# Performance work log

Measured on AMD Instinct MI355X. Metric: run time of the kernel, lower is better.

The kernel has to match this reference:

```python
import jax, jax.numpy as jnp
import numpy as np

N, E, B, C, L, HLS = 30000, 480000, 64, 128, 3, 64
PARAM_NAMES = ['Wq','bq','Wk','bk','Wv','bv','Wskip','bskip','lstm_Wih_f','lstm_Whh_f','lstm_bih_f','lstm_bhh_f','lstm_Wih_b','lstm_Whh_b','lstm_bih_b','lstm_bhh_b','att_W','att_b','gP_W1','gP_b1','gP_W2','gP_b2','gT_W1','gT_b1','gT_W2','gT_b2','m_W0','m_b0','m_W1','m_b1','m_W2','m_b2']


def setup_inputs() -> dict:
    key = jax.random.key(0)
    ks = iter(jax.random.split(key, 64))
    rn = lambda shape: jax.random.normal(next(ks), shape, dtype=jnp.float32) * 0.05
    inp = {
        'x': jax.random.normal(next(ks), (N, C), dtype=jnp.float32),
        'edge_index': jax.random.randint(next(ks), (2, E), 0, N, dtype=jnp.int32),
        'batch': jnp.sort(jax.random.randint(next(ks), (N,), 0, B, dtype=jnp.int32)),
        'hls_attr': jax.random.normal(next(ks), (B, HLS), dtype=jnp.float32),
        'Wq': rn((L, C, C)), 'bq': rn((L, C)),
        'Wk': rn((L, C, C)), 'bk': rn((L, C)),
        'Wv': rn((L, C, C)), 'bv': rn((L, C)),
        'Wskip': rn((L, C, C)), 'bskip': rn((L, C)),
        'lstm_Wih_f': rn((4 * C, C)), 'lstm_Whh_f': rn((4 * C, C)),
        'lstm_bih_f': rn((4 * C,)), 'lstm_bhh_f': rn((4 * C,)),
        'lstm_Wih_b': rn((4 * C, C)), 'lstm_Whh_b': rn((4 * C, C)),
        'lstm_bih_b': rn((4 * C,)), 'lstm_bhh_b': rn((4 * C,)),
        'att_W': rn((2 * C, 1)), 'att_b': rn((1,)),
        'gP_W1': rn((C, C)), 'gP_b1': rn((C,)), 'gP_W2': rn((C, 1)), 'gP_b2': rn((1,)),
        'gT_W1': rn((C, C)), 'gT_b1': rn((C,)), 'gT_W2': rn((C, 1)), 'gT_b2': rn((1,)),
        'm_W0': rn((2 * C + HLS, 64)), 'm_b0': rn((64,)),
        'm_W1': rn((64, 64)), 'm_b1': rn((64,)),
        'm_W2': rn((64, 1)), 'm_b2': rn((1,)),
    }
    return inp


def _segment_softmax(logits, seg, num):
    m = jax.ops.segment_max(logits, seg, num_segments=num)
    e = jnp.exp(logits - m[seg])
    d = jax.ops.segment_sum(e, seg, num_segments=num)
    return e / d[seg]


def _lstm(xs, Wih, Whh, bih, bhh):
    # xs: [L, N, C] -> outputs [L, N, H]
    H = Whh.shape[1]
    h0 = jnp.zeros((xs.shape[1], H), xs.dtype)
    bias = bih + bhh
    def step(carry, xt):
        h, c = carry
        z = xt @ Wih.T + h @ Whh.T + bias
        i, f, g, o = jnp.split(z, 4, axis=-1)
        c = jax.nn.sigmoid(f) * c + jax.nn.sigmoid(i) * jnp.tanh(g)
        h = jax.nn.sigmoid(o) * jnp.tanh(c)
        return (h, c), h
    _, hs = jax.lax.scan(step, (h0, h0), xs)
    return hs


def _gate_pool(x, batch, W1, b1, W2, b2):
    gate = jax.nn.relu(x @ W1 + b1) @ W2 + b2          # [N, 1]
    gate = _segment_softmax(gate[:, 0], batch, B)[:, None]
    return jax.ops.segment_sum(gate * x, batch, num_segments=B)


def _forward(x, edge_index, batch, hls_attr, Wq, bq, Wk, bk, Wv, bv, Wskip, bskip,
             lstm_Wih_f, lstm_Whh_f, lstm_bih_f, lstm_bhh_f,
             lstm_Wih_b, lstm_Whh_b, lstm_bih_b, lstm_bhh_b,
             att_W, att_b, gP_W1, gP_b1, gP_W2, gP_b2, gT_W1, gT_b1, gT_W2, gT_b2,
             m_W0, m_b0, m_W1, m_b1, m_W2, m_b2):
    src, dst = edge_index[0], edge_index[1]
    scale = 1.0 / jnp.sqrt(jnp.asarray(C, jnp.float32))
    h_list = []
    for i in range(L):
        q = x @ Wq[i] + bq[i]
        k = x @ Wk[i] + bk[i]
        v = x @ Wv[i] + bv[i]
        logits = jnp.sum(q[dst] * k[src], axis=-1) * scale   # [E]
        alpha = _segment_softmax(logits, dst, N)             # per-dst softmax
        agg = jax.ops.segment_sum(alpha[:, None] * v[src], dst, num_segments=N)
        x = jax.nn.relu(agg + x @ Wskip[i] + bskip[i])       # TransformerConv + root skip, then ReLU
        h_list.append(x)
    xs = jnp.stack(h_list)                                   # [L, N, C]
    hf = _lstm(xs, lstm_Wih_f, lstm_Whh_f, lstm_bih_f, lstm_bhh_f)
    hb = _lstm(xs[::-1], lstm_Wih_b, lstm_Whh_b, lstm_bih_b, lstm_bhh_b)[::-1]
    hcat = jnp.concatenate([hf, hb], axis=-1)                # [L, N, 2C]
    a = jax.nn.softmax((hcat @ att_W)[..., 0] + att_b[0], axis=0)  # softmax over layers
    x = jnp.sum(a[..., None] * xs, axis=0)                   # [N, C] JK-LSTM output
    out_P = _gate_pool(x, batch, gP_W1, gP_b1, gP_W2, gP_b2)
    out_T = _gate_pool(x, batch, gT_W1, gT_b1, gT_W2, gT_b2)
    h = jnp.concatenate([out_P, out_T, hls_attr], axis=-1)   # [B, 2C+HLS]
    h = jax.nn.relu(h @ m_W0 + m_b0)
    h = jax.nn.relu(h @ m_W1 + m_b1)
    return h @ m_W2 + m_b2                                   # [B, 1]


def reference(x, edge_index, batch, hls_attr, Wq, bq, Wk, bk, Wv, bv, Wskip, bskip,
              lstm_Wih_f, lstm_Whh_f, lstm_bih_f, lstm_bhh_f,
              lstm_Wih_b, lstm_Whh_b, lstm_bih_b, lstm_bhh_b,
              att_W, att_b, gP_W1, gP_b1, gP_W2, gP_b2, gT_W1, gT_b1, gT_W2, gT_b2,
              m_W0, m_b0, m_W1, m_b1, m_W2, m_b2):
    return _forward(x, edge_index, batch, hls_attr, Wq, bq, Wk, bk, Wv, bv, Wskip, bskip,
                    lstm_Wih_f, lstm_Whh_f, lstm_bih_f, lstm_bhh_f,
                    lstm_Wih_b, lstm_Whh_b, lstm_bih_b, lstm_bhh_b,
                    att_W, att_b, gP_W1, gP_b1, gP_W2, gP_b2, gT_W1, gT_b1, gT_W2, gT_b2,
                    m_W0, m_b0, m_W1, m_b1, m_W2, m_b2)
```

## Files before the change

### kernel.cpp

```cpp
#include <hip/hip_runtime.h>
#include <math.h>

#define NN 30000
#define EE 480000
#define BB 64
#define CC 128
#define LLAYERS 3
#define HLSD 64

typedef __attribute__((ext_vector_type(8))) short bf16x8;
typedef __attribute__((ext_vector_type(4))) float f32x4;

__device__ inline unsigned short f2bf(float f){
  unsigned u = __float_as_uint(f);
  u += 0x7fffu + ((u >> 16) & 1u);
  return (unsigned short)(u >> 16);
}
__device__ inline float bf2f(unsigned short h){
  return __uint_as_float(((unsigned)h) << 16);
}

__global__ void k_hist(const int* __restrict__ dst, int* __restrict__ counts, int E){
  int e = blockIdx.x*256 + threadIdx.x;
  if (e < E) atomicAdd(&counts[dst[e]], 1);
}
__global__ void k_scan_block(const int* __restrict__ counts, int* __restrict__ row_ptr,
                             int* __restrict__ bsums, int n){
  __shared__ int sm[256];
  int i = blockIdx.x*256 + threadIdx.x;
  int v = (i < n) ? counts[i] : 0;
  sm[threadIdx.x] = v; __syncthreads();
  for (int off = 1; off < 256; off <<= 1){
    int t = (threadIdx.x >= off) ? sm[threadIdx.x - off] : 0;
    __syncthreads();
    sm[threadIdx.x] += t;
    __syncthreads();
  }
  if (i < n) row_ptr[i+1] = sm[threadIdx.x];
  if (threadIdx.x == 255) bsums[blockIdx.x] = sm[255];
}
__global__ void k_scan_bsums(const int* __restrict__ bsums, int* __restrict__ bexcl, int nb){
  if (threadIdx.x == 0 && blockIdx.x == 0){
    int s = 0;
    for (int i = 0; i < nb; i++){ int t = bsums[i]; bexcl[i] = s; s += t; }
  }
}
__global__ void k_scan_add(int* __restrict__ row_ptr, const int* __restrict__ bexcl, int n){
  int i = blockIdx.x*256 + threadIdx.x;
  if (i < n) row_ptr[i+1] += bexcl[i >> 8];
  if (i == 0) row_ptr[0] = 0;
}
__global__ void k_fill(const int* __restrict__ src, const int* __restrict__ dst,
                       const int* __restrict__ row_ptr, int* __restrict__ fill,
                       int* __restrict__ esrc, int E){
  int e = blockIdx.x*256 + threadIdx.x;
  if (e < E){
    int d = dst[e];
    int pos = row_ptr[d] + atomicAdd(&fill[d], 1);
    esrc[pos] = src[e];
  }
}

struct PrepPtrs {
  const float* tsrc[14]; unsigned short* tdst[14];
  const float* csrc[4];  unsigned short* cdst[4];
  const float *bihf, *bhhf, *bihb, *bhhb;
  float *cbf, *cbb;
};
__global__ __launch_bounds__(256) void k_prep(PrepPtrs p){
  int b = blockIdx.x, tid = threadIdx.x;
  if (b < 14){
    const float* s = p.tsrc[b]; unsigned short* d = p.tdst[b];
    for (int i = tid; i < 16384; i += 256){
      int k = i >> 7, n = i & 127;
      d[n*128 + k] = f2bf(s[i]);
    }
  } else if (b < 30){
    int m = (b - 14) >> 2, ch = (b - 14) & 3;
    const float* s = p.csrc[m] + ch*16384; unsigned short* d = p.cdst[m] + ch*16384;
    for (int i = tid; i < 16384; i += 256) d[i] = f2bf(s[i]);
  } else {
    for (int i = tid; i < 512; i += 256){
      p.cbf[i] = p.bihf[i] + p.bhhf[i];
      p.cbb[i] = p.bihb[i] + p.bhhb[i];
    }
  }
}
__global__ __launch_bounds__(256) void k_cvt_x(const float* __restrict__ src,
                                               unsigned short* __restrict__ dst, int n8){
  int i = blockIdx.x*256 + threadIdx.x;
  if (i >= n8) return;
  float4 a = *(const float4*)(src + (size_t)i*8);
  float4 b = *(const float4*)(src + (size_t)i*8 + 4);
  union { unsigned short u[8]; uint4 v; } o;
  o.u[0]=f2bf(a.x); o.u[1]=f2bf(a.y); o.u[2]=f2bf(a.z); o.u[3]=f2bf(a.w);
  o.u[4]=f2bf(b.x); o.u[5]=f2bf(b.y); o.u[6]=f2bf(b.z); o.u[7]=f2bf(b.w);
  *(uint4*)(dst + (size_t)i*8) = o.v;
}

struct Quad { const unsigned short* Bt[4]; const float* bias[4]; };

template<int RELU, int OUTBF16>
__global__ __launch_bounds__(256) void k_mfma_gemm(
    const unsigned short* __restrict__ A0, Quad qd,
    float* __restrict__ Cf, unsigned short* __restrict__ Cb,
    int M, int ldC, int colsPerMat)
{
  __shared__ unsigned short As0[64*128];
  __shared__ unsigned short Bs0[64*128];

  const int tid = threadIdx.x;
  const int row0 = blockIdx.x*64;
  const int colg0 = blockIdx.y*64;
  const int mi = colg0 / colsPerMat;
  const int nloc = colg0 - mi*colsPerMat;
  const unsigned short* Bt0 = qd.Bt[mi];

  #pragma unroll
  for (int i = 0; i < 4; i++){
    int ch = tid + i*256;
    int r = ch >> 4, c16 = ch & 15;
    int gr = row0 + r;
    uint4 av = make_uint4(0,0,0,0);
    if (gr < M) av = *(const uint4*)(A0 + (size_t)gr*128 + c16*8);
    *(uint4*)((char*)As0 + ((r*256 + c16*16) ^ ((r&7)<<4))) = av;
    uint4 bv = *(const uint4*)(Bt0 + (size_t)(nloc + r)*128 + c16*8);
    *(uint4*)((char*)Bs0 + ((r*256 + c16*16) ^ ((r&7)<<4))) = bv;
  }
  __syncthreads();

  const int w = tid >> 6, l = tid & 63;
  const int lr = l & 15, lhi = l >> 4;

  f32x4 acc[4];
  #pragma unroll
  for (int f = 0; f < 4; f++){ acc[f][0]=0.f; acc[f][1]=0.f; acc[f][2]=0.f; acc[f][3]=0.f; }

  #pragma unroll
  for (int kt = 0; kt < 4; kt++){
    int arow = w*16 + lr;
    bf16x8 a = *(const bf16x8*)((const char*)As0 + ((arow*256 + kt*64 + lhi*16) ^ ((arow&7)<<4)));
    #pragma unroll
    for (int f = 0; f < 4; f++){
      int brow = f*16 + lr;
      bf16x8 b = *(const bf16x8*)((const char*)Bs0 + ((brow*256 + kt*64 + lhi*16) ^ ((brow&7)<<4)));
      acc[f] = __builtin_amdgcn_mfma_f32_16x16x32_bf16(a, b, acc[f], 0, 0, 0);
    }
  }

  const float* bias = qd.bias[mi];
  #pragma unroll
  for (int f = 0; f < 4; f++){
    int colg = colg0 + f*16 + lr;
    float bv = bias ? bias[nloc + f*16 + lr] : 0.f;
    #pragma unroll
    for (int r = 0; r < 4; r++){
      int grow = row0 + w*16 + lhi*4 + r;
      if (grow < M){
        float v = acc[f][r] + bv;
        if (RELU) v = fmaxf(v, 0.f);
        if (OUTBF16) Cb[(size_t)grow*ldC + colg] = f2bf(v);
        else         Cf[(size_t)grow*ldC + colg] = v;
      }
    }
  }
}

template<int FIRST>
__global__ __launch_bounds__(256) void k_lstm_fused(
    const unsigned short* __restrict__ X,
    const unsigned short* __restrict__ H,
    const unsigned short* __restrict__ Wih,
    const unsigned short* __restrict__ Whh,
    const float* __restrict__ cbias,
    unsigned short* __restrict__ Hout,
    float* __restrict__ Cst,
    float* __restrict__ score,
    const float* __restrict__ attW,
    int M)
{
  __shared__ unsigned short As[64*128];
  __shared__ unsigned short Bs[128*128];
  const int tid = threadIdx.x;
  const int row0 = blockIdx.x*64;
  const int t0 = blockIdx.y*32;
  const int w = tid >> 6, l = tid & 63, lr = l & 15, lhi = l >> 4;

  f32x4 acc[8];
  #pragma unroll
  for (int f = 0; f < 8; f++){ acc[f][0]=0.f; acc[f][1]=0.f; acc[f][2]=0.f; acc[f][3]=0.f; }

  const int npair = FIRST ? 1 : 2;
  for (int pair = 0; pair < npair; pair++){
    const unsigned short* A  = pair ? H   : X;
    const unsigned short* Bt = pair ? Whh : Wih;
    if (pair) __syncthreads();
    #pragma unroll
    for (int i = 0; i < 4; i++){
      int ch = tid + i*256;
      int r = ch >> 4, c16 = ch & 15;
      int gr = row0 + r;
      uint4 av = make_uint4(0,0,0,0);
      if (gr < M) av = *(const uint4*)(A + (size_t)gr*128 + c16*8);
      *(uint4*)((char*)As + ((r*256 + c16*16) ^ ((r&7)<<4))) = av;
    }
    #pragma unroll
    for (int i = 0; i < 8; i++){
      int ch = tid + i*256;
      int r = ch >> 4, c16 = ch & 15;
      int gr = (r >> 5)*128 + t0 + (r & 31);
      uint4 bv = *(const uint4*)(Bt + (size_t)gr*128 + c16*8);
      *(uint4*)((char*)Bs + ((r*256 + c16*16) ^ ((r&7)<<4))) = bv;
    }
    __syncthreads();
    #pragma unroll
    for (int kt = 0; kt < 4; kt++){
      int arow = w*16 + lr;
      bf16x8 a = *(const bf16x8*)((const char*)As + ((arow*256 + kt*64 + lhi*16) ^ ((arow&7)<<4)));
      #pragma unroll
      for (int f = 0; f < 8; f++){
        int brow = f*16 + lr;
        bf16x8 b = *(const bf16x8*)((const char*)Bs + ((brow*256 + kt*64 + lhi*16) ^ ((brow&7)<<4)));
        acc[f] = __builtin_amdgcn_mfma_f32_16x16x32_bf16(a, b, acc[f], 0, 0, 0);
      }
    }
  }

  float sc[4] = {0.f, 0.f, 0.f, 0.f};
  #pragma unroll
  for (int cb = 0; cb < 2; cb++){
    int t = t0 + cb*16 + lr;
    float aw  = attW[t];
    float bi  = cbias[t];
    float bf_ = cbias[128 + t];
    float bg  = cbias[256 + t];
    float bo  = cbias[384 + t];
    #pragma unroll
    for (int r = 0; r < 4; r++){
      int grow = row0 + w*16 + lhi*4 + r;
      if (grow < M){
        float zi = acc[0+cb][r] + bi;
        float zf = acc[2+cb][r] + bf_;
        float zg = acc[4+cb][r] + bg;
        float zo = acc[6+cb][r] + bo;
        float cp = FIRST ? 0.f : Cst[(size_t)grow*128 + t];
        float si = 1.f/(1.f + expf(-zi));
        float sf = 1.f/(1.f + expf(-zf));
        float so = 1.f/(1.f + expf(-zo));
        float cn = sf*cp + si*tanhf(zg);
        float hn = so*tanhf(cn);
        Cst[(size_t)grow*128 + t] = cn;
        Hout[(size_t)grow*128 + t] = f2bf(hn);
        sc[r] += hn * aw;
      }
    }
  }
  #pragma unroll
  for (int r = 0; r < 4; r++){
    float p = sc[r];
    p += __shfl_xor(p, 1, 64);
    p += __shfl_xor(p, 2, 64);
    p += __shfl_xor(p, 4, 64);
    p += __shfl_xor(p, 8, 64);
    if (lr == 0){
      int grow = row0 + w*16 + lhi*4 + r;
      if (grow < M) atomicAdd(&score[grow], p);
    }
  }
}

__global__ __launch_bounds__(256) void k_attn(
    const unsigned short* __restrict__ qkvs, const int* __restrict__ row_ptr,
    const int* __restrict__ esrc, unsigned short* __restrict__ xout, int n)
{
  int wid = threadIdx.x >> 6, lane = threadIdx.x & 63;
  int dst = blockIdx.x*4 + wid;
  if (dst >= n) return;
  const size_t drow = (size_t)dst*512;
  ushort2 qu = *(const ushort2*)(qkvs + drow + lane*2);
  float qx = bf2f(qu.x), qy = bf2f(qu.y);
  int rs = row_ptr[dst], re = row_ptr[dst+1];
  const float scale = 0.08838834764831845f;
  float m = -INFINITY, den = 0.f, ax = 0.f, ay = 0.f;
  int e = rs;
  for (; e + 4 <= re; e += 4){
    int s0 = esrc[e], s1 = esrc[e+1], s2 = esrc[e+2], s3 = esrc[e+3];
    const unsigned short* r0 = qkvs + (size_t)s0*512;
    const unsigned short* r1 = qkvs + (size_t)s1*512;
    const unsigned short* r2 = qkvs + (size_t)s2*512;
    const unsigned short* r3 = qkvs + (size_t)s3*512;
    ushort2 k0 = *(const ushort2*)(r0 + 128 + lane*2);
    ushort2 k1 = *(const ushort2*)(r1 + 128 + lane*2);
    ushort2 k2 = *(const ushort2*)(r2 + 128 + lane*2);
    ushort2 k3 = *(const ushort2*)(r3 + 128 + lane*2);
    ushort2 v0 = *(const ushort2*)(r0 + 256 + lane*2);
    ushort2 v1 = *(const ushort2*)(r1 + 256 + lane*2);
    ushort2 v2 = *(const ushort2*)(r2 + 256 + lane*2);
    ushort2 v3 = *(const ushort2*)(r3 + 256 + lane*2);
    float d0 = qx*bf2f(k0.x) + qy*bf2f(k0.y);
    float d1 = qx*bf2f(k1.x) + qy*bf2f(k1.y);
    float d2 = qx*bf2f(k2.x) + qy*bf2f(k2.y);
    float d3 = qx*bf2f(k3.x) + qy*bf2f(k3.y);
    #pragma unroll
    for (int o = 1; o < 64; o <<= 1){
      d0 += __shfl_xor(d0, o, 64);
      d1 += __shfl_xor(d1, o, 64);
      d2 += __shfl_xor(d2, o, 64);
      d3 += __shfl_xor(d3, o, 64);
    }
    float l0 = d0*scale, l1 = d1*scale, l2 = d2*scale, l3 = d3*scale;
    float bm = fmaxf(fmaxf(l0, l1), fmaxf(l2, l3));
    if (bm > m){
      float rr = expf(m - bm);
      den *= rr; ax *= rr; ay *= rr; m = bm;
    }
    float w0 = expf(l0 - m), w1 = expf(l1 - m), w2 = expf(l2 - m), w3 = expf(l3 - m);
    den += (w0 + w1) + (w2 + w3);
    ax += w0*bf2f(v0.x) + w1*bf2f(v1.x) + w2*bf2f(v2.x) + w3*bf2f(v3.x);
    ay += w0*bf2f(v0.y) + w1*bf2f(v1.y) + w2*bf2f(v2.y) + w3*bf2f(v3.y);
  }
  for (; e < re; ++e){
    int s = esrc[e];
    const unsigned short* sr = qkvs + (size_t)s*512;
    ushort2 kk = *(const ushort2*)(sr + 128 + lane*2);
    ushort2 vv = *(const ushort2*)(sr + 256 + lane*2);
    float d = qx*bf2f(kk.x) + qy*bf2f(kk.y);
    #pragma unroll
    for (int o = 1; o < 64; o <<= 1) d += __shfl_xor(d, o, 64);
    float logit = d * scale;
    if (logit > m){
      float rr = expf(m - logit);
      den *= rr; ax *= rr; ay *= rr; m = logit;
    }
    float wgt = expf(logit - m);
    den += wgt; ax += wgt*bf2f(vv.x); ay += wgt*bf2f(vv.y);
  }
  ushort2 sku = *(const ushort2*)(qkvs + drow + 384 + lane*2);
  float ox = 0.f, oy = 0.f;
  if (re > rs){ ox = ax/den; oy = ay/den; }
  ox = fmaxf(ox + bf2f(sku.x), 0.f); oy = fmaxf(oy + bf2f(sku.y), 0.f);
  ushort2 o2; o2.x = f2bf(ox); o2.y = f2bf(oy);
  *(ushort2*)(xout + (size_t)dst*128 + lane*2) = o2;
}

__global__ void k_jk_weights(const float* __restrict__ sF, const float* __restrict__ sB,
                             const float* __restrict__ attb, float* __restrict__ a, int n){
  int i = blockIdx.x*256 + threadIdx.x;
  if (i >= n) return;
  float s0 = sF[i]       + sB[i]       + attb[0];
  float s1 = sF[n+i]     + sB[n+i]     + attb[0];
  float s2 = sF[2*n+i]   + sB[2*n+i]   + attb[0];
  float mm = fmaxf(s0, fmaxf(s1, s2));
  float e0 = expf(s0-mm), e1 = expf(s1-mm), e2 = expf(s2-mm);
  float d = e0 + e1 + e2;
  a[i] = e0/d; a[n+i] = e1/d; a[2*n+i] = e2/d;
}
__global__ void k_jk_combine(const float* __restrict__ a,
                             const unsigned short* __restrict__ x0,
                             const unsigned short* __restrict__ x1,
                             const unsigned short* __restrict__ x2,
                             float* __restrict__ xjk, unsigned short* __restrict__ xjkb, int n){
  int idx = blockIdx.x*256 + threadIdx.x;
  if (idx >= n*128) return;
  int node = idx >> 7;
  float r = a[node]     * bf2f(x0[idx])
          + a[n+node]   * bf2f(x1[idx])
          + a[2*n+node] * bf2f(x2[idx]);
  xjk[idx] = r;
  xjkb[idx] = f2bf(r);
}

__global__ __launch_bounds__(256) void k_rowdot(const unsigned short* __restrict__ g,
                                                const float* __restrict__ w2,
                                                const float* __restrict__ b2, float* __restrict__ out, int n){
  int wid = threadIdx.x >> 6, lane = threadIdx.x & 63;
  int node = blockIdx.x*4 + wid;
  if (node >= n) return;
  ushort2 gv = *(const ushort2*)(g + (size_t)node*128 + lane*2);
  float2 wv = *(const float2*)(w2 + lane*2);
  float p = bf2f(gv.x)*wv.x + bf2f(gv.y)*wv.y;
  #pragma unroll
  for (int o = 1; o < 64; o <<= 1) p += __shfl_xor(p, o, 64);
  if (lane == 0) out[node] = p + b2[0];
}

__global__ void k_segbounds(const int* __restrict__ batch, int* __restrict__ segp, int n){
  int i = blockIdx.x*256 + threadIdx.x;
  if (i >= n) return;
  int b = batch[i];
  int bp = (i == 0) ? -1 : batch[i-1];
  for (int s = bp+1; s <= b; s++) segp[s] = i;
  if (i == n-1){
    for (int s = b+1; s <= BB; s++) segp[s] = n;
  }
}

__global__ __launch_bounds__(256) void k_seg_stats(
    const float* __restrict__ glP, const float* __restrict__ glT,
    const int* __restrict__ segp, float4* __restrict__ stats)
{
  const int b = blockIdx.x, tid = threadIdx.x;
  const int s0 = segp[b], s1 = segp[b+1];
  __shared__ float sred[8];

  float mP = -INFINITY, mT = -INFINITY;
  for (int i = s0 + tid; i < s1; i += 256){
    mP = fmaxf(mP, glP[i]);
    mT = fmaxf(mT, glT[i]);
  }
  #pragma unroll
  for (int o = 1; o < 64; o <<= 1){
    mP = fmaxf(mP, __shfl_xor(mP, o, 64));
    mT = fmaxf(mT, __shfl_xor(mT, o, 64));
  }
  if ((tid & 63) == 0){ sred[(tid >> 6)*2] = mP; sred[(tid >> 6)*2 + 1] = mT; }
  __syncthreads();
  mP = fmaxf(fmaxf(sred[0], sred[2]), fmaxf(sred[4], sred[6]));
  mT = fmaxf(fmaxf(sred[1], sred[3]), fmaxf(sred[5], sred[7]));
  __syncthreads();

  float dP = 0.f, dT = 0.f;
  for (int i = s0 + tid; i < s1; i += 256){
    dP += expf(glP[i] - mP);
    dT += expf(glT[i] - mT);
  }
  #pragma unroll
  for (int o = 1; o < 64; o <<= 1){
    dP += __shfl_xor(dP, o, 64);
    dT += __shfl_xor(dT, o, 64);
  }
  if ((tid & 63) == 0){ sred[(tid >> 6)*2] = dP; sred[(tid >> 6)*2 + 1] = dT; }
  __syncthreads();
  if (tid == 0){
    dP = sred[0] + sred[2] + sred[4] + sred[6];
    dT = sred[1] + sred[3] + sred[5] + sred[7];
    float4 st;
    st.x = mP; st.y = mT;
    st.z = (dP > 0.f) ? 1.f/dP : 0.f;
    st.w = (dT > 0.f) ? 1.f/dT : 0.f;
    stats[b] = st;
  }
}

__global__ __launch_bounds__(256) void k_poolsum(
    const float* __restrict__ xjk, const int* __restrict__ segp,
    const float* __restrict__ glP, const float* __restrict__ glT,
    const float4* __restrict__ stats,
    float* __restrict__ poolP, float* __restrict__ poolT)
{
  const int b = blockIdx.x;
  const int s0 = segp[b], s1 = segp[b+1];
  const float4 st = stats[b];
  const int half = threadIdx.x >> 7, c = threadIdx.x & 127;
  const int stream = blockIdx.y*2 + half;
  float aP = 0.f, aT = 0.f;
  for (int i = s0 + stream; i < s1; i += 32){
    float eP = expf(glP[i] - st.x);
    float eT = expf(glT[i] - st.y);
    float xv = xjk[(size_t)i*128 + c];
    aP += eP*xv; aT += eT*xv;
  }
  if (aP != 0.f) atomicAdd(&poolP[(size_t)b*128 + c], aP*st.z);
  if (aT != 0.f) atomicAdd(&poolT[(size_t)b*128 + c], aT*st.w);
}

__global__ __launch_bounds__(64) void k_mlp(
    const float* __restrict__ poolP, const float* __restrict__ poolT, const float* __restrict__ hls,
    const float* __restrict__ W0, const float* __restrict__ b0,
    const float* __restrict__ W1, const float* __restrict__ b1,
    const float* __restrict__ W2, const float* __restrict__ b2, float* __restrict__ out)
{
  __shared__ float hin[320];
  __shared__ float h1[64];
  int b = blockIdx.x, j = threadIdx.x;
  for (int i = j; i < 320; i += 64){
    float vv;
    if (i < 128)      vv = poolP[(size_t)b*128 + i];
    else if (i < 256) vv = poolT[(size_t)b*128 + (i-128)];
    else              vv = hls[(size_t)b*64 + (i-256)];
    hin[i] = vv;
  }
  __syncthreads();
  float s = b0[j];
  for (int kk = 0; kk < 320; kk++) s += hin[kk] * W0[kk*64 + j];
  h1[j] = fmaxf(s, 0.f);
  __syncthreads();
  float s2 = b1[j];
  for (int kk = 0; kk < 64; kk++) s2 += h1[kk] * W1[kk*64 + j];
  float h2 = fmaxf(s2, 0.f);
  float p = h2 * W2[j];
  #pragma unroll
  for (int o = 1; o < 64; o <<= 1) p += __shfl_xor(p, o, 64);
  if (j == 0) out[b] = p + b2[0];
}

extern "C" void kernel_launch(void* const* d_in, const int* in_sizes, int n_in,
                              void* d_out, int out_size, void* d_ws, size_t ws_size,
                              hipStream_t stream)
{
  (void)in_sizes; (void)n_in; (void)out_size; (void)ws_size;
  const int N = NN, E = EE, C = CC;
  const float* x     = (const float*)d_in[0];
  const int*   ei    = (const int*)d_in[1];
  const int*   batch = (const int*)d_in[2];
  const float* hls   = (const float*)d_in[3];
  const float* Wq = (const float*)d_in[4],  *bq = (const float*)d_in[5];
  const float* Wk = (const float*)d_in[6],  *bk = (const float*)d_in[7];
  const float* Wv = (const float*)d_in[8],  *bv = (const float*)d_in[9];
  const float* Ws = (const float*)d_in[10], *bs = (const float*)d_in[11];
  const float* Wih_f = (const float*)d_in[12], *Whh_f = (const float*)d_in[13];
  const float* bih_f = (const float*)d_in[14], *bhh_f = (const float*)d_in[15];
  const float* Wih_b = (const float*)d_in[16], *Whh_b = (const float*)d_in[17];
  const float* bih_b = (const float*)d_in[18], *bhh_b = (const float*)d_in[19];
  const float* attW  = (const float*)d_in[20], *attb  = (const float*)d_in[21];
  const float* gPW1 = (const float*)d_in[22], *gPb1 = (const float*)d_in[23];
  const float* gPW2 = (const float*)d_in[24], *gPb2 = (const float*)d_in[25];
  const float* gTW1 = (const float*)d_in[26], *gTb1 = (const float*)d_in[27];
  const float* gTW2 = (const float*)d_in[28], *gTb2 = (const float*)d_in[29];
  const float* mW0 = (const float*)d_in[30], *mb0 = (const float*)d_in[31];
  const float* mW1 = (const float*)d_in[32], *mb1 = (const float*)d_in[33];
  const float* mW2 = (const float*)d_in[34], *mb2 = (const float*)d_in[35];
  float* out = (float*)d_out;

  const int* esrc_in = ei;
  const int* edst_in = ei + E;

  typedef unsigned short u16;

  char* ws = (char*)d_ws;
  size_t off = 0;
  auto alloc = [&](size_t bytes) -> char* {
    char* p = ws + off;
    off += (bytes + 255) & ~(size_t)255;
    return p;
  };
  u16* qkvsb   = (u16*)alloc((size_t)N*512*2);
  u16* xb      = (u16*)alloc((size_t)N*C*2);
  u16* xsb0    = (u16*)alloc((size_t)N*C*2);
  u16* xsb1    = (u16*)alloc((size_t)N*C*2);
  u16* xsb2    = (u16*)alloc((size_t)N*C*2);
  u16* hbA     = (u16*)alloc((size_t)N*C*2);
  u16* hbB     = (u16*)alloc((size_t)N*C*2);
  float* cbuf  = (float*)alloc((size_t)N*C*4);
  float* scores= (float*)alloc((size_t)6*N*4);
  float* ajk   = (float*)alloc((size_t)3*N*4);
  float* xjk   = (float*)alloc((size_t)N*C*4);
  u16* xjkb    = (u16*)alloc((size_t)N*C*2);
  u16* g1P     = (u16*)alloc((size_t)N*C*2);
  u16* g1T     = (u16*)alloc((size_t)N*C*2);
  int* counts  = (int*)alloc((size_t)N*4);
  int* row_ptr = (int*)alloc((size_t)(N+1)*4);
  int* bsums   = (int*)alloc(512);
  int* bexcl   = (int*)alloc(512);
  int* esrc    = (int*)alloc((size_t)E*4);
  float* glP   = (float*)alloc((size_t)N*4);
  float* glT   = (float*)alloc((size_t)N*4);
  int* segp    = (int*)alloc((size_t)(BB+1)*4);
  float* poolP = (float*)alloc((size_t)BB*C*4);
  float* poolT = (float*)alloc((size_t)BB*C*4);
  float4* sstats = (float4*)alloc((size_t)BB*16);
  u16* wT      = (u16*)alloc((size_t)14*16384*2);
  u16* wLSTM   = (u16*)alloc((size_t)4*65536*2);
  float* combF = (float*)alloc(512*4);
  float* combB = (float*)alloc(512*4);

  float* scF = scores;
  float* scB = scores + (size_t)3*N;

  u16* wTq = wT;
  u16* wTk = wT + 3*16384;
  u16* wTv = wT + 6*16384;
  u16* wTs = wT + 9*16384;
  u16* wTgP = wT + 12*16384;
  u16* wTgT = wT + 13*16384;
  u16* wIHf = wLSTM;
  u16* wHHf = wLSTM + 65536;
  u16* wIHb = wLSTM + 2*65536;
  u16* wHHb = wLSTM + 3*65536;

  const int NB  = (N + 255)/256;
  const int EBL = (E + 255)/256;

  PrepPtrs pp;
  for (int l = 0; l < 3; l++){
    pp.tsrc[l]   = Wq + (size_t)l*16384;  pp.tdst[l]   = wTq + (size_t)l*16384;
    pp.tsrc[3+l] = Wk + (size_t)l*16384;  pp.tdst[3+l] = wTk + (size_t)l*16384;
    pp.tsrc[6+l] = Wv + (size_t)l*16384;  pp.tdst[6+l] = wTv + (size_t)l*16384;
    pp.tsrc[9+l] = Ws + (size_t)l*16384;  pp.tdst[9+l] = wTs + (size_t)l*16384;
  }
  pp.tsrc[12] = gPW1; pp.tdst[12] = wTgP;
  pp.tsrc[13] = gTW1; pp.tdst[13] = wTgT;
  pp.csrc[0] = Wih_f; pp.cdst[0] = wIHf;
  pp.csrc[1] = Whh_f; pp.cdst[1] = wHHf;
  pp.csrc[2] = Wih_b; pp.cdst[2] = wIHb;
  pp.csrc[3] = Whh_b; pp.cdst[3] = wHHb;
  pp.bihf = bih_f; pp.bhhf = bhh_f; pp.bihb = bih_b; pp.bhhb = bhh_b;
  pp.cbf = combF; pp.cbb = combB;
  k_prep<<<31, 256, 0, stream>>>(pp);
  k_cvt_x<<<(N*C/8 + 255)/256, 256, 0, stream>>>(x, xb, N*C/8);

  hipMemsetAsync(counts, 0, (size_t)N*4, stream);
  k_hist<<<EBL, 256, 0, stream>>>(edst_in, counts, E);
  k_scan_block<<<NB, 256, 0, stream>>>(counts, row_ptr, bsums, N);
  k_scan_bsums<<<1, 64, 0, stream>>>(bsums, bexcl, NB);
  k_scan_add<<<NB, 256, 0, stream>>>(row_ptr, bexcl, N);
  hipMemsetAsync(counts, 0, (size_t)N*4, stream);
  k_fill<<<EBL, 256, 0, stream>>>(esrc_in, edst_in, row_ptr, counts, esrc, E);

  const int GX = (N + 63)/64;
  dim3 blk(256);

  u16* xsb[3] = {xsb0, xsb1, xsb2};
  const u16* ain = xb;
  for (int l = 0; l < LLAYERS; l++){
    Quad q;
    q.Bt[0] = wTq + (size_t)l*16384;  q.bias[0] = bq + (size_t)l*C;
    q.Bt[1] = wTk + (size_t)l*16384;  q.bias[1] = bk + (size_t)l*C;
    q.Bt[2] = wTv + (size_t)l*16384;  q.bias[2] = bv + (size_t)l*C;
    q.Bt[3] = wTs + (size_t)l*16384;  q.bias[3] = bs + (size_t)l*C;
    k_mfma_gemm<0,1><<<dim3(GX,8), blk, 0, stream>>>(ain, q, nullptr, qkvsb, N, 512, 128);
    k_attn<<<(N+3)/4, 256, 0, stream>>>(qkvsb, row_ptr, esrc, xsb[l], N);
    ain = xsb[l];
  }

  hipMemsetAsync(scores, 0, (size_t)6*N*4, stream);
  {
    u16* hbuf2[2] = {hbA, hbB};
    for (int t = 0; t < 3; t++){
      u16* hout = hbuf2[t & 1];
      u16* hin2 = hbuf2[(t & 1) ^ 1];
      if (t == 0)
        k_lstm_fused<1><<<dim3(GX,4), blk, 0, stream>>>(xsb[t], nullptr, wIHf, nullptr, combF,
                                                        hout, cbuf, scF + (size_t)t*N, attW, N);
      else
        k_lstm_fused<0><<<dim3(GX,4), blk, 0, stream>>>(xsb[t], hin2, wIHf, wHHf, combF,
                                                        hout, cbuf, scF + (size_t)t*N, attW, N);
    }
    for (int s = 0; s < 3; s++){
      int t = 2 - s;
      u16* hout = hbuf2[s & 1];
      u16* hin2 = hbuf2[(s & 1) ^ 1];
      if (s == 0)
        k_lstm_fused<1><<<dim3(GX,4), blk, 0, stream>>>(xsb[t], nullptr, wIHb, nullptr, combB,
                                                        hout, cbuf, scB + (size_t)t*N, attW + 128, N);
      else
        k_lstm_fused<0><<<dim3(GX,4), blk, 0, stream>>>(xsb[t], hin2, wIHb, wHHb, combB,
                                                        hout, cbuf, scB + (size_t)t*N, attW + 128, N);
    }
  }

  k_jk_weights<<<NB, 256, 0, stream>>>(scF, scB, attb, ajk, N);
  k_jk_combine<<<(N*C + 255)/256, 256, 0, stream>>>(ajk, xsb0, xsb1, xsb2, xjk, xjkb, N);

  {
    Quad qp; qp.Bt[0]=wTgP; qp.bias[0]=gPb1; qp.Bt[1]=nullptr; qp.bias[1]=nullptr; qp.Bt[2]=nullptr; qp.bias[2]=nullptr; qp.Bt[3]=nullptr; qp.bias[3]=nullptr;
    k_mfma_gemm<1,1><<<dim3(GX,2), blk, 0, stream>>>(xjkb, qp, nullptr, g1P, N, 128, 128);
    k_rowdot<<<(N+3)/4, 256, 0, stream>>>(g1P, gPW2, gPb2, glP, N);
    Quad qt; qt.Bt[0]=wTgT; qt.bias[0]=gTb1; qt.Bt[1]=nullptr; qt.bias[1]=nullptr; qt.Bt[2]=nullptr; qt.bias[2]=nullptr; qt.Bt[3]=nullptr; qt.bias[3]=nullptr;
    k_mfma_gemm<1,1><<<dim3(GX,2), blk, 0, stream>>>(xjkb, qt, nullptr, g1T, N, 128, 128);
    k_rowdot<<<(N+3)/4, 256, 0, stream>>>(g1T, gTW2, gTb2, glT, N);
  }

  k_segbounds<<<NB, 256, 0, stream>>>(batch, segp, N);
  k_seg_stats<<<BB, 256, 0, stream>>>(glP, glT, segp, sstats);
  hipMemsetAsync(poolP, 0, (size_t)2*BB*C*4, stream);
  k_poolsum<<<dim3(BB,16), 256, 0, stream>>>(xjk, segp, glP, glT, sstats, poolP, poolT);

  k_mlp<<<BB, 64, 0, stream>>>(poolP, poolT, hls, mW0, mb0, mW1, mb1, mW2, mb2, out);
}
```

Measured before the change: 545.4 us.

## Split attention wavefront into four edge groups with 16-byte vector loads

The per-destination attention kernel now splits each 64-lane wavefront into four 16-lane groups. Each group handles every fourth edge, with each lane loading 8 bf16 channels in one 16-byte access. Each group keeps its own online softmax state, software-prefetches the next edge's K/V rows, uses exp2 with a prescaled logit, and merges the partial softmax states across groups with shuffles at the end. This cuts the dot-product shuffle reduction from 6 steps to 4 per edge and issues wider memory accesses, at the cost of more registers and a cross-group merge.

```diff
diff --git a/kernel.cpp b/kernel.cpp
--- a/kernel.cpp
+++ b/kernel.cpp
@@ -276,71 +276,85 @@
   int wid = threadIdx.x >> 6, lane = threadIdx.x & 63;
   int dst = blockIdx.x*4 + wid;
   if (dst >= n) return;
+  const int g = lane >> 4, j = lane & 15;
   const size_t drow = (size_t)dst*512;
-  ushort2 qu = *(const ushort2*)(qkvs + drow + lane*2);
-  float qx = bf2f(qu.x), qy = bf2f(qu.y);
-  int rs = row_ptr[dst], re = row_ptr[dst+1];
-  const float scale = 0.08838834764831845f;
-  float m = -INFINITY, den = 0.f, ax = 0.f, ay = 0.f;
-  int e = rs;
-  for (; e + 4 <= re; e += 4){
-    int s0 = esrc[e], s1 = esrc[e+1], s2 = esrc[e+2], s3 = esrc[e+3];
-    const unsigned short* r0 = qkvs + (size_t)s0*512;
-    const unsigned short* r1 = qkvs + (size_t)s1*512;
-    const unsigned short* r2 = qkvs + (size_t)s2*512;
-    const unsigned short* r3 = qkvs + (size_t)s3*512;
-    ushort2 k0 = *(const ushort2*)(r0 + 128 + lane*2);
-    ushort2 k1 = *(const ushort2*)(r1 + 128 + lane*2);
-    ushort2 k2 = *(const ushort2*)(r2 + 128 + lane*2);
-    ushort2 k3 = *(const ushort2*)(r3 + 128 + lane*2);
-    ushort2 v0 = *(const ushort2*)(r0 + 256 + lane*2);
-    ushort2 v1 = *(const ushort2*)(r1 + 256 + lane*2);
-    ushort2 v2 = *(const ushort2*)(r2 + 256 + lane*2);
-    ushort2 v3 = *(const ushort2*)(r3 + 256 + lane*2);
-    float d0 = qx*bf2f(k0.x) + qy*bf2f(k0.y);
-    float d1 = qx*bf2f(k1.x) + qy*bf2f(k1.y);
-    float d2 = qx*bf2f(k2.x) + qy*bf2f(k2.y);
-    float d3 = qx*bf2f(k3.x) + qy*bf2f(k3.y);
-    #pragma unroll
-    for (int o = 1; o < 64; o <<= 1){
-      d0 += __shfl_xor(d0, o, 64);
-      d1 += __shfl_xor(d1, o, 64);
-      d2 += __shfl_xor(d2, o, 64);
-      d3 += __shfl_xor(d3, o, 64);
-    }
-    float l0 = d0*scale, l1 = d1*scale, l2 = d2*scale, l3 = d3*scale;
-    float bm = fmaxf(fmaxf(l0, l1), fmaxf(l2, l3));
-    if (bm > m){
-      float rr = expf(m - bm);
-      den *= rr; ax *= rr; ay *= rr; m = bm;
-    }
-    float w0 = expf(l0 - m), w1 = expf(l1 - m), w2 = expf(l2 - m), w3 = expf(l3 - m);
-    den += (w0 + w1) + (w2 + w3);
-    ax += w0*bf2f(v0.x) + w1*bf2f(v1.x) + w2*bf2f(v2.x) + w3*bf2f(v3.x);
-    ay += w0*bf2f(v0.y) + w1*bf2f(v1.y) + w2*bf2f(v2.y) + w3*bf2f(v3.y);
-  }
-  for (; e < re; ++e){
+
+  bf16x8 qv = *(const bf16x8*)(qkvs + drow + j*8);
+  float qf[8];
+  #pragma unroll
+  for (int i = 0; i < 8; i++) qf[i] = bf2f((unsigned short)qv[i]);
+
+  const int rs = row_ptr[dst], re = row_ptr[dst+1];
+  const float scale2 = 0.08838834764831845f * 1.4426950408889634f;
+  float m = -INFINITY, den = 0.f;
+  float acc[8];
+  #pragma unroll
+  for (int i = 0; i < 8; i++) acc[i] = 0.f;
+
+  int e = rs + g;
+  if (e < re){
     int s = esrc[e];
-    const unsigned short* sr = qkvs + (size_t)s*512;
-    ushort2 kk = *(const ushort2*)(sr + 128 + lane*2);
-    ushort2 vv = *(const ushort2*)(sr + 256 + lane*2);
-    float d = qx*bf2f(kk.x) + qy*bf2f(kk.y);
-    #pragma unroll
-    for (int o = 1; o < 64; o <<= 1) d += __shfl_xor(d, o, 64);
-    float logit = d * scale;
-    if (logit > m){
-      float rr = expf(m - logit);
-      den *= rr; ax *= rr; ay *= rr; m = logit;
-    }
-    float wgt = expf(logit - m);
-    den += wgt; ax += wgt*bf2f(vv.x); ay += wgt*bf2f(vv.y);
-  }
-  ushort2 sku = *(const ushort2*)(qkvs + drow + 384 + lane*2);
-  float ox = 0.f, oy = 0.f;
-  if (re > rs){ ox = ax/den; oy = ay/den; }
-  ox = fmaxf(ox + bf2f(sku.x), 0.f); oy = fmaxf(oy + bf2f(sku.y), 0.f);
-  ushort2 o2; o2.x = f2bf(ox); o2.y = f2bf(oy);
-  *(ushort2*)(xout + (size_t)dst*128 + lane*2) = o2;
+    const unsigned short* sr = qkvs + (size_t)s*512 + j*8;
+    bf16x8 kc = *(const bf16x8*)(sr + 128);
+    bf16x8 vc = *(const bf16x8*)(sr + 256);
+    while (true){
+      int en = e + 4;
+      bool havenext = en < re;
+      bf16x8 kn, vn;
+      if (havenext){
+        int sn = esrc[en];
+        const unsigned short* srn = qkvs + (size_t)sn*512 + j*8;
+        kn = *(const bf16x8*)(srn + 128);
+        vn = *(const bf16x8*)(srn + 256);
+      }
+      float d = qf[0]*bf2f((unsigned short)kc[0]);
+      #pragma unroll
+      for (int i = 1; i < 8; i++) d += qf[i]*bf2f((unsigned short)kc[i]);
+      d += __shfl_xor(d, 1, 64);
+      d += __shfl_xor(d, 2, 64);
+      d += __shfl_xor(d, 4, 64);
+      d += __shfl_xor(d, 8, 64);
+      float logit = d * scale2;
+      float mn = fmaxf(m, logit);
+      float rr = exp2f(m - mn);
+      float wgt = exp2f(logit - mn);
+      den = den*rr + wgt;
+      #pragma unroll
+      for (int i = 0; i < 8; i++)
+        acc[i] = acc[i]*rr + wgt*bf2f((unsigned short)vc[i]);
+      m = mn;
+      if (!havenext) break;
+      e = en; kc = kn; vc = vn;
+    }
+  }
+
+  #pragma unroll
+  for (int o = 16; o <= 32; o <<= 1){
+    float mo  = __shfl_xor(m, o, 64);
+    float dno = __shfl_xor(den, o, 64);
+    float mn  = fmaxf(m, mo);
+    float ss  = (m  > -INFINITY) ? exp2f(m  - mn) : 0.f;
+    float so  = (mo > -INFINITY) ? exp2f(mo - mn) : 0.f;
+    den = den*ss + dno*so;
+    #pragma unroll
+    for (int i = 0; i < 8; i++){
+      float ao = __shfl_xor(acc[i], o, 64);
+      acc[i] = acc[i]*ss + ao*so;
+    }
+    m = mn;
+  }
+
+  if (g == 0){
+    bf16x8 sk = *(const bf16x8*)(qkvs + drow + 384 + j*8);
+    float inv = (re > rs) ? 1.f/den : 0.f;
+    union { unsigned short u[8]; uint4 v; } o8;
+    #pragma unroll
+    for (int i = 0; i < 8; i++){
+      float v = acc[i]*inv + bf2f((unsigned short)sk[i]);
+      o8.u[i] = f2bf(fmaxf(v, 0.f));
+    }
+    *(uint4*)(xout + (size_t)dst*128 + j*8) = o8.v;
+  }
 }
 
 __global__ void k_jk_weights(const float* __restrict__ sF, const float* __restrict__ sB,
```

New measurement: 524.5 us. 3.8% less time.
